# Optimization experiments

Hardware: AMD Instinct MI355X
Metric: run time of the kernel (lower is better)

Reference implementation:

```python
import jax, jax.numpy as jnp
import numpy as np

N_NODES = 100000
N_EDGES = 1600000
HIDDEN = 128
N_FILTERS = 64
CUTOFF = 8.0
BN_EPS = 1e-3  # keras BatchNormalization default epsilon


def setup_inputs() -> dict:
    key = jax.random.key(0)
    ks = jax.random.split(key, 12)
    x = jax.random.normal(ks[0], (N_NODES, HIDDEN), dtype=jnp.float32)
    edge_index = jax.random.randint(ks[1], (2, N_EDGES), 0, N_NODES, dtype=jnp.int32)
    edge_weight = jax.random.uniform(ks[2], (N_EDGES,), dtype=jnp.float32) * CUTOFF
    edge_attr = jax.random.uniform(ks[3], (N_EDGES, 1), dtype=jnp.float32)
    s = 0.05
    # filter_net: Dense(1->64, tanh), Dense(64->64)
    Wf1 = jax.random.normal(ks[4], (1, N_FILTERS), dtype=jnp.float32) * s
    bf1 = jnp.zeros((N_FILTERS,), jnp.float32)
    Wf2 = jax.random.normal(ks[5], (N_FILTERS, N_FILTERS), dtype=jnp.float32) * s
    bf2 = jnp.zeros((N_FILTERS,), jnp.float32)
    # interaction_net: Dense(128->128, softplus), Dense(128->128)
    Wi1 = jax.random.normal(ks[6], (HIDDEN, HIDDEN), dtype=jnp.float32) * s
    bi1 = jnp.zeros((HIDDEN,), jnp.float32)
    Wi2 = jax.random.normal(ks[7], (HIDDEN, HIDDEN), dtype=jnp.float32) * s
    bi2 = jnp.zeros((HIDDEN,), jnp.float32)
    # BatchNormalization (inference: moving stats)
    gamma = jnp.ones((HIDDEN,), jnp.float32)
    beta = jnp.zeros((HIDDEN,), jnp.float32)
    mov_mean = jax.random.normal(ks[8], (HIDDEN,), dtype=jnp.float32) * 0.01
    mov_var = jnp.ones((HIDDEN,), jnp.float32)
    return {"x": x, "edge_index": edge_index, "edge_weight": edge_weight,
            "edge_attr": edge_attr, "Wf1": Wf1, "bf1": bf1, "Wf2": Wf2, "bf2": bf2,
            "Wi1": Wi1, "bi1": bi1, "Wi2": Wi2, "bi2": bi2,
            "gamma": gamma, "beta": beta, "mov_mean": mov_mean, "mov_var": mov_var}


def reference(x, edge_index, edge_weight, edge_attr, Wf1, bf1, Wf2, bf2,
              Wi1, bi1, Wi2, bi2, gamma, beta, mov_mean, mov_var):
    row, col = edge_index[0], edge_index[1]
    # continuous filters with smooth cosine cutoff
    scaled = edge_weight * (2.0 / CUTOFF) - 1.0                    # [E]
    h = jnp.tanh(scaled[:, None] @ Wf1 + bf1)                      # [E, F]
    filters = h @ Wf2 + bf2                                        # [E, F]
    cut = 0.5 * (jnp.cos(edge_weight * jnp.pi / CUTOFF) + 1.0)
    cut = jnp.where(edge_weight <= CUTOFF, cut, 0.0)               # [E]
    filters = filters * cut[:, None]
    # Original: (neighbor[:, None, :] * filters[:, :, None]).sum(axis=1)
    # == neighbor * filters.sum(-1, keepdims) — same math, no [E,F,H] tensor.
    fsum = jnp.sum(filters, axis=-1, keepdims=True)                # [E, 1]
    messages = x[col] * fsum                                       # [E, H]
    agg = jax.ops.segment_sum(messages, row, num_segments=x.shape[0])  # [N, H]
    out = jax.nn.softplus(agg @ Wi1 + bi1) @ Wi2 + bi2             # [N, H]
    # BatchNormalization, inference mode (training=False)
    out = gamma * (out - mov_mean) * jax.lax.rsqrt(mov_var + BN_EPS) + beta
    return out
```

## Files before the change

### kernel.cpp

```cpp
#include <hip/hip_runtime.h>
#include <math.h>

#define HIDDEN 128
#define NFILT 64
#define SCAN_B 1024
#define LUTK 2048

typedef __attribute__((ext_vector_type(8))) short bf16x8;
typedef __attribute__((ext_vector_type(4))) float f32x4;

__device__ __forceinline__ short f2bf(float f) {
    unsigned u = __float_as_uint(f);
    unsigned r = (u + 0x7fffu + ((u >> 16) & 1u)) >> 16;
    return (short)r;
}
__device__ __forceinline__ float bf2f(unsigned short u) {
    return __uint_as_float(((unsigned)u) << 16);
}

__device__ __forceinline__ float softplus_fast(float v) {
    float e = __builtin_amdgcn_exp2f(v * 1.4426950408889634f);
    float r = 0.69314718055994531f * __builtin_amdgcn_logf(1.0f + e);
    return (v > 80.f) ? v : r;
}

__global__ void wsum_kernel(const float* __restrict__ Wf2, const float* __restrict__ bf2,
                            float* __restrict__ wsum, float* __restrict__ bsum) {
    int j = threadIdx.x;
    float s = 0.f;
    for (int f = 0; f < NFILT; ++f) s += Wf2[j * NFILT + f];
    wsum[j] = s;
    if (j == 0) {
        float b = 0.f;
        for (int f = 0; f < NFILT; ++f) b += bf2[f];
        *bsum = b;
    }
}

__device__ __forceinline__ float edge_coeff(float w,
                                            const float* sW, const float* sB,
                                            const float* sS, float bsum) {
    float s = fmaf(w, 0.25f, -1.0f);
    float acc = bsum;
    #pragma unroll 8
    for (int j = 0; j < NFILT; ++j)
        acc += tanhf(fmaf(s, sW[j], sB[j])) * sS[j];
    float cut = (w <= 8.0f) ? 0.5f * (cosf(w * 0.39269908169872414f) + 1.0f) : 0.0f;
    return acc * cut;
}

__global__ void lut_kernel(const float* __restrict__ Wf1, const float* __restrict__ bf1,
                           const float* __restrict__ wsum, const float* __restrict__ bsum,
                           float* __restrict__ lut) {
    int i = blockIdx.x * 256 + threadIdx.x;
    if (i > LUTK) return;
    float w = 8.0f * (float)i / (float)LUTK;
    lut[i] = edge_coeff(w, Wf1, bf1, wsum, *bsum);
}

__device__ __forceinline__ float lut_eval(const float* sl, float w) {
    float t = w * ((float)LUTK / 8.0f);
    t = fminf(fmaxf(t, 0.f), (float)LUTK);
    int i = (int)t;
    i = min(i, LUTK - 1);
    return fmaf(t - (float)i, sl[i + 1] - sl[i], sl[i]);
}

__global__ void prep_w_kernel(const float* __restrict__ Wi1, const float* __restrict__ Wi2,
                              short* __restrict__ W1T, short* __restrict__ W2T) {
    int idx = blockIdx.x * 256 + threadIdx.x;
    const float* src = (idx < 16384) ? Wi1 : Wi2;
    short* dst = (idx < 16384) ? W1T : W2T;
    int i = idx & 16383;
    int k = i >> 7, n = i & 127;
    dst[n * HIDDEN + k] = f2bf(src[i]);
}

__global__ void prep_bn_kernel(const float* __restrict__ bi2,
                               const float* __restrict__ gamma, const float* __restrict__ beta,
                               const float* __restrict__ mean, const float* __restrict__ var,
                               float* __restrict__ scf, float* __restrict__ shf) {
    int j = threadIdx.x;
    float sc = gamma[j] * rsqrtf(var[j] + 1e-3f);
    scf[j] = sc;
    shf[j] = (bi2[j] - mean[j]) * sc + beta[j];
}

__global__ void x2bf_kernel(const float* __restrict__ x, short* __restrict__ xh, int total8) {
    int i = blockIdx.x * 256 + threadIdx.x;
    if (i >= total8) return;
    const float4 v0 = *(const float4*)&x[(size_t)i * 8];
    const float4 v1 = *(const float4*)&x[(size_t)i * 8 + 4];
    bf16x8 o;
    o[0] = f2bf(v0.x); o[1] = f2bf(v0.y); o[2] = f2bf(v0.z); o[3] = f2bf(v0.w);
    o[4] = f2bf(v1.x); o[5] = f2bf(v1.y); o[6] = f2bf(v1.z); o[7] = f2bf(v1.w);
    *(bf16x8*)&xh[(size_t)i * 8] = o;
}

__global__ void count_rank_kernel(const int* __restrict__ rows, int* __restrict__ deg,
                                  int* __restrict__ rank, int E) {
    int e = blockIdx.x * blockDim.x + threadIdx.x;
    if (e < E) rank[e] = atomicAdd(&deg[rows[e]], 1);
}

__global__ void count_kernel(const int* __restrict__ rows, int* __restrict__ deg, int E) {
    int e = blockIdx.x * blockDim.x + threadIdx.x;
    if (e < E) atomicAdd(&deg[rows[e]], 1);
}

__global__ __launch_bounds__(SCAN_B) void scan_p1(const int* __restrict__ deg,
                                                  int* __restrict__ bsums, int N) {
    __shared__ int red[SCAN_B];
    int i = blockIdx.x * SCAN_B + threadIdx.x;
    red[threadIdx.x] = (i < N) ? deg[i] : 0;
    __syncthreads();
    for (int off = SCAN_B / 2; off > 0; off >>= 1) {
        if (threadIdx.x < off) red[threadIdx.x] += red[threadIdx.x + off];
        __syncthreads();
    }
    if (threadIdx.x == 0) bsums[blockIdx.x] = red[0];
}

__global__ __launch_bounds__(SCAN_B) void scan_p2(int* __restrict__ bsums, int B) {
    __shared__ int part[SCAN_B];
    int t = threadIdx.x;
    part[t] = (t < B) ? bsums[t] : 0;
    __syncthreads();
    for (int off = 1; off < SCAN_B; off <<= 1) {
        int v = (t >= off) ? part[t - off] : 0;
        __syncthreads();
        part[t] += v;
        __syncthreads();
    }
    if (t < B) bsums[t] = (t == 0) ? 0 : part[t - 1];
}

template <bool WRITE_CURSOR>
__global__ __launch_bounds__(SCAN_B) void scan_p3_t(int* __restrict__ deg,
                                                    const int* __restrict__ bsums,
                                                    int* __restrict__ offs, int N) {
    __shared__ int part[SCAN_B];
    int t = threadIdx.x;
    int i = blockIdx.x * SCAN_B + t;
    int d = (i < N) ? deg[i] : 0;
    part[t] = d;
    __syncthreads();
    for (int off = 1; off < SCAN_B; off <<= 1) {
        int v = (t >= off) ? part[t - off] : 0;
        __syncthreads();
        part[t] += v;
        __syncthreads();
    }
    int pre = bsums[blockIdx.x] + part[t] - d;
    if (i < N) {
        offs[i] = pre;
        if (WRITE_CURSOR) deg[i] = pre;
        if (i == N - 1) offs[N] = pre + d;
    }
}

__global__ __launch_bounds__(256) void fill_rank_kernel(
    const int* __restrict__ rows, const int* __restrict__ cols,
    const float* __restrict__ ew, const int* __restrict__ rank,
    const int* __restrict__ offs, const float* __restrict__ lut,
    int2* __restrict__ epack, int E) {
    __shared__ float sl[LUTK + 1];
    for (int i = threadIdx.x; i <= LUTK; i += 256) sl[i] = lut[i];
    __syncthreads();
    int e = blockIdx.x * 256 + threadIdx.x;
    if (e >= E) return;
    float f = lut_eval(sl, ew[e]);
    int pos = offs[rows[e]] + rank[e];
    epack[pos] = make_int2(cols[e], __float_as_int(f));
}

__global__ __launch_bounds__(256) void fill_cursor_kernel(
    const int* __restrict__ rows, const int* __restrict__ cols,
    const float* __restrict__ ew, int* __restrict__ cursor,
    const float* __restrict__ lut, int2* __restrict__ epack, int E) {
    __shared__ float sl[LUTK + 1];
    for (int i = threadIdx.x; i <= LUTK; i += 256) sl[i] = lut[i];
    __syncthreads();
    int e = blockIdx.x * 256 + threadIdx.x;
    if (e >= E) return;
    float f = lut_eval(sl, ew[e]);
    int pos = atomicAdd(&cursor[rows[e]], 1);
    epack[pos] = make_int2(cols[e], __float_as_int(f));
}

__global__ __launch_bounds__(256) void gather_bf_kernel(const int* __restrict__ offs,
                                                        const int2* __restrict__ epack,
                                                        const short* __restrict__ xh,
                                                        short* __restrict__ aggh, int N) {
    int t = threadIdx.x;
    int node = blockIdx.x * 8 + (t >> 5);
    if (node >= N) return;
    int lane = t & 31;
    int s = offs[node], eend = offs[node + 1];
    float a0 = 0.f, a1 = 0.f, a2 = 0.f, a3 = 0.f;

    int i = s;
    for (; i + 4 <= eend; i += 4) {
        int2 p0 = epack[i];
        int2 p1 = epack[i + 1];
        int2 p2 = epack[i + 2];
        int2 p3 = epack[i + 3];
        ushort4 x0 = *(const ushort4*)&xh[(size_t)p0.x * HIDDEN + lane * 4];
        ushort4 x1 = *(const ushort4*)&xh[(size_t)p1.x * HIDDEN + lane * 4];
        ushort4 x2 = *(const ushort4*)&xh[(size_t)p2.x * HIDDEN + lane * 4];
        ushort4 x3 = *(const ushort4*)&xh[(size_t)p3.x * HIDDEN + lane * 4];
        float f0 = __int_as_float(p0.y), f1 = __int_as_float(p1.y);
        float f2 = __int_as_float(p2.y), f3 = __int_as_float(p3.y);
        a0 = fmaf(bf2f(x0.x), f0, a0); a1 = fmaf(bf2f(x0.y), f0, a1);
        a2 = fmaf(bf2f(x0.z), f0, a2); a3 = fmaf(bf2f(x0.w), f0, a3);
        a0 = fmaf(bf2f(x1.x), f1, a0); a1 = fmaf(bf2f(x1.y), f1, a1);
        a2 = fmaf(bf2f(x1.z), f1, a2); a3 = fmaf(bf2f(x1.w), f1, a3);
        a0 = fmaf(bf2f(x2.x), f2, a0); a1 = fmaf(bf2f(x2.y), f2, a1);
        a2 = fmaf(bf2f(x2.z), f2, a2); a3 = fmaf(bf2f(x2.w), f2, a3);
        a0 = fmaf(bf2f(x3.x), f3, a0); a1 = fmaf(bf2f(x3.y), f3, a1);
        a2 = fmaf(bf2f(x3.z), f3, a2); a3 = fmaf(bf2f(x3.w), f3, a3);
    }
    for (; i < eend; ++i) {
        int2 p = epack[i];
        float f = __int_as_float(p.y);
        ushort4 xv = *(const ushort4*)&xh[(size_t)p.x * HIDDEN + lane * 4];
        a0 = fmaf(bf2f(xv.x), f, a0);
        a1 = fmaf(bf2f(xv.y), f, a1);
        a2 = fmaf(bf2f(xv.z), f, a2);
        a3 = fmaf(bf2f(xv.w), f, a3);
    }
    ushort4 o;
    o.x = (unsigned short)f2bf(a0);
    o.y = (unsigned short)f2bf(a1);
    o.z = (unsigned short)f2bf(a2);
    o.w = (unsigned short)f2bf(a3);
    *(ushort4*)&aggh[(size_t)node * HIDDEN + lane * 4] = o;
}

__global__ __launch_bounds__(256) void gather_kernel(const int* __restrict__ offs,
                                                     const int2* __restrict__ epack,
                                                     const float* __restrict__ x,
                                                     float* __restrict__ agg, int N) {
    int t = threadIdx.x;
    int node = blockIdx.x * 8 + (t >> 5);
    if (node >= N) return;
    int lane = t & 31;
    int s = offs[node], eend = offs[node + 1];
    float4 acc = make_float4(0.f, 0.f, 0.f, 0.f);
    int i = s;
    for (; i + 2 <= eend; i += 2) {
        int2 p0 = epack[i];
        int2 p1 = epack[i + 1];
        float4 x0 = *(const float4*)&x[(size_t)p0.x * HIDDEN + lane * 4];
        float4 x1 = *(const float4*)&x[(size_t)p1.x * HIDDEN + lane * 4];
        float f0 = __int_as_float(p0.y), f1 = __int_as_float(p1.y);
        acc.x = fmaf(x0.x, f0, acc.x); acc.y = fmaf(x0.y, f0, acc.y);
        acc.z = fmaf(x0.z, f0, acc.z); acc.w = fmaf(x0.w, f0, acc.w);
        acc.x = fmaf(x1.x, f1, acc.x); acc.y = fmaf(x1.y, f1, acc.y);
        acc.z = fmaf(x1.z, f1, acc.z); acc.w = fmaf(x1.w, f1, acc.w);
    }
    for (; i < eend; ++i) {
        int2 p = epack[i];
        float f = __int_as_float(p.y);
        const float4 xv = *(const float4*)&x[(size_t)p.x * HIDDEN + lane * 4];
        acc.x = fmaf(xv.x, f, acc.x);
        acc.y = fmaf(xv.y, f, acc.y);
        acc.z = fmaf(xv.z, f, acc.z);
        acc.w = fmaf(xv.w, f, acc.w);
    }
    *(float4*)&agg[(size_t)node * HIDDEN + lane * 4] = acc;
}

#define HROW 136

#define WSWZ(b) ((b) ^ ((((b) >> 8) & 7) << 4))

__global__ __launch_bounds__(512) void mlp_mfma_bf_kernel(
    const short* __restrict__ aggh, float* __restrict__ io,
    const short* __restrict__ W1T, const short* __restrict__ W2T,
    const float* __restrict__ bi1,
    const float* __restrict__ scf, const float* __restrict__ shf,
    int N) {
    __shared__ short wS[HIDDEN * HIDDEN];
    __shared__ short hS[128 * HROW];

    const int t = threadIdx.x;
    const int wave = t >> 6;
    const int lane = t & 63;
    const int quad = lane >> 4;
    const int m16  = lane & 15;
    const int row0 = blockIdx.x * 128 + wave * 16;
    const int arow = row0 + m16;

    const int swzmask = (m16 & 7) << 4;

    bf16x8 w2r[4];
    {
        const bf16x8* w1v = (const bf16x8*)W1T;
        const bf16x8* w2v = (const bf16x8*)W2T;
        bf16x8 w1r[4];
        #pragma unroll
        for (int j = 0; j < 4; ++j) w1r[j] = w1v[t + 512 * j];
        #pragma unroll
        for (int j = 0; j < 4; ++j) w2r[j] = w2v[t + 512 * j];
        #pragma unroll
        for (int j = 0; j < 4; ++j) {
            int b = (t + 512 * j) * 16;
            *(bf16x8*)((char*)wS + WSWZ(b)) = w1r[j];
        }
    }

    float b1v[8];
    #pragma unroll
    for (int ct = 0; ct < 8; ++ct) b1v[ct] = bi1[ct * 16 + m16];

    f32x4 acc[8];
    #pragma unroll
    for (int ct = 0; ct < 8; ++ct) acc[ct] = (f32x4)(0.f);

    __syncthreads();

    #pragma unroll
    for (int ks = 0; ks < 4; ++ks) {
        bf16x8 a;
        if (arow < N) {
            a = *(const bf16x8*)&aggh[(size_t)arow * HIDDEN + ks * 32 + quad * 8];
        } else {
            #pragma unroll
            for (int j = 0; j < 8; ++j) a[j] = 0;
        }
        const char* bbase = (const char*)wS + m16 * 256 + ((ks * 64 + quad * 16) ^ swzmask);
        #pragma unroll
        for (int ct = 0; ct < 8; ++ct) {
            bf16x8 b = *(const bf16x8*)(bbase + ct * 4096);
            acc[ct] = __builtin_amdgcn_mfma_f32_16x16x32_bf16(a, b, acc[ct], 0, 0, 0);
        }
    }

    #pragma unroll
    for (int ct = 0; ct < 8; ++ct) {
        int col = ct * 16 + m16;
        #pragma unroll
        for (int r = 0; r < 4; ++r) {
            int lrow = wave * 16 + quad * 4 + r;
            float h = softplus_fast(acc[ct][r] + b1v[ct]);
            hS[lrow * HROW + col] = f2bf(h);
        }
        acc[ct] = (f32x4)(0.f);
    }
    __syncthreads();

    #pragma unroll
    for (int j = 0; j < 4; ++j) {
        int b = (t + 512 * j) * 16;
        *(bf16x8*)((char*)wS + WSWZ(b)) = w2r[j];
    }
    __syncthreads();

    float scv[8], shv[8];
    #pragma unroll
    for (int ct = 0; ct < 8; ++ct) {
        scv[ct] = scf[ct * 16 + m16];
        shv[ct] = shf[ct * 16 + m16];
    }

    #pragma unroll
    for (int ks = 0; ks < 4; ++ks) {
        bf16x8 a = *(const bf16x8*)&hS[(wave * 16 + m16) * HROW + ks * 32 + quad * 8];
        const char* bbase = (const char*)wS + m16 * 256 + ((ks * 64 + quad * 16) ^ swzmask);
        #pragma unroll
        for (int ct = 0; ct < 8; ++ct) {
            bf16x8 b = *(const bf16x8*)(bbase + ct * 4096);
            acc[ct] = __builtin_amdgcn_mfma_f32_16x16x32_bf16(a, b, acc[ct], 0, 0, 0);
        }
    }

    #pragma unroll
    for (int r = 0; r < 4; ++r) {
        int grow = row0 + quad * 4 + r;
        if (grow < N) {
            float* p = &io[(size_t)grow * HIDDEN + m16];
            #pragma unroll
            for (int ct = 0; ct < 8; ++ct)
                p[ct * 16] = fmaf(acc[ct][r], scv[ct], shv[ct]);
        }
    }
}

__global__ __launch_bounds__(256) void mlp_mfma_kernel(
    float* io,
    const short* __restrict__ W1T, const short* __restrict__ W2T,
    const float* __restrict__ bi1,
    const float* __restrict__ scf, const float* __restrict__ shf,
    int N) {
    __shared__ short hS[64 * HROW];

    const int t = threadIdx.x;
    const int wave = t >> 6;
    const int lane = t & 63;
    const int quad = lane >> 4;
    const int m16  = lane & 15;
    const int row0 = blockIdx.x * 64 + wave * 16;
    const int arow = row0 + m16;

    f32x4 acc[8];
    #pragma unroll
    for (int ct = 0; ct < 8; ++ct) acc[ct] = (f32x4)(0.f);

    #pragma unroll
    for (int ks = 0; ks < 4; ++ks) {
        bf16x8 a;
        if (arow < N) {
            const float* ap = &io[(size_t)arow * HIDDEN + ks * 32 + quad * 8];
            float4 v0 = *(const float4*)ap;
            float4 v1 = *(const float4*)(ap + 4);
            a[0] = f2bf(v0.x); a[1] = f2bf(v0.y); a[2] = f2bf(v0.z); a[3] = f2bf(v0.w);
            a[4] = f2bf(v1.x); a[5] = f2bf(v1.y); a[6] = f2bf(v1.z); a[7] = f2bf(v1.w);
        } else {
            #pragma unroll
            for (int j = 0; j < 8; ++j) a[j] = 0;
        }
        #pragma unroll
        for (int ct = 0; ct < 8; ++ct) {
            bf16x8 b = *(const bf16x8*)&W1T[(ct * 16 + m16) * HIDDEN + ks * 32 + quad * 8];
            acc[ct] = __builtin_amdgcn_mfma_f32_16x16x32_bf16(a, b, acc[ct], 0, 0, 0);
        }
    }

    #pragma unroll
    for (int ct = 0; ct < 8; ++ct) {
        int col = ct * 16 + m16;
        float b1 = bi1[col];
        #pragma unroll
        for (int r = 0; r < 4; ++r) {
            int lrow = wave * 16 + quad * 4 + r;
            float h = softplus_fast(acc[ct][r] + b1);
            hS[lrow * HROW + col] = f2bf(h);
            acc[ct][r] = 0.f;
        }
    }
    __syncthreads();

    #pragma unroll
    for (int ks = 0; ks < 4; ++ks) {
        bf16x8 a = *(const bf16x8*)&hS[(wave * 16 + m16) * HROW + ks * 32 + quad * 8];
        #pragma unroll
        for (int ct = 0; ct < 8; ++ct) {
            bf16x8 b = *(const bf16x8*)&W2T[(ct * 16 + m16) * HIDDEN + ks * 32 + quad * 8];
            acc[ct] = __builtin_amdgcn_mfma_f32_16x16x32_bf16(a, b, acc[ct], 0, 0, 0);
        }
    }

    #pragma unroll
    for (int ct = 0; ct < 8; ++ct) {
        int col = ct * 16 + m16;
        float sc = scf[col], sh = shf[col];
        #pragma unroll
        for (int r = 0; r < 4; ++r) {
            int grow = row0 + quad * 4 + r;
            if (grow < N)
                io[(size_t)grow * HIDDEN + col] = fmaf(acc[ct][r], sc, sh);
        }
    }
}

__global__ void edge_filter_kernel(const float* __restrict__ ew,
                                   const float* __restrict__ Wf1, const float* __restrict__ bf1,
                                   const float* __restrict__ wsum, const float* __restrict__ bsum,
                                   float* __restrict__ fs, int E) {
    __shared__ float sW[NFILT], sB[NFILT], sS[NFILT];
    if (threadIdx.x < NFILT) {
        sW[threadIdx.x] = Wf1[threadIdx.x];
        sB[threadIdx.x] = bf1[threadIdx.x];
        sS[threadIdx.x] = wsum[threadIdx.x];
    }
    __syncthreads();
    int e = blockIdx.x * blockDim.x + threadIdx.x;
    if (e >= E) return;
    fs[e] = edge_coeff(ew[e], sW, sB, sS, *bsum);
}

__global__ void scatter_kernel(const int* __restrict__ rows, const int* __restrict__ cols,
                               const float* __restrict__ x, const float* __restrict__ fs,
                               float* __restrict__ agg, int E) {
    int t = threadIdx.x;
    int e = blockIdx.x * 8 + (t >> 5);
    if (e >= E) return;
    int lane = t & 31;
    int r = rows[e];
    int c = cols[e];
    float f = fs[e];
    const float4 xv = *(const float4*)&x[c * HIDDEN + lane * 4];
    float* dst = &agg[r * HIDDEN + lane * 4];
    atomicAdd(dst + 0, xv.x * f);
    atomicAdd(dst + 1, xv.y * f);
    atomicAdd(dst + 2, xv.z * f);
    atomicAdd(dst + 3, xv.w * f);
}

__global__ __launch_bounds__(256) void mlp_kernel(
    float* __restrict__ io,
    const float* __restrict__ Wi1, const float* __restrict__ bi1,
    const float* __restrict__ Wi2, const float* __restrict__ bi2,
    const float* __restrict__ gamma, const float* __restrict__ beta,
    const float* __restrict__ mean, const float* __restrict__ var,
    int N) {
    __shared__ float As[64 * HIDDEN];
    __shared__ float Wh[64 * HIDDEN];

    const int t = threadIdx.x;
    const int row0 = blockIdx.x * 64;
    const int col4 = (t & 31) * 4;
    const int rgrp = t >> 5;

    #pragma unroll
    for (int i = 0; i < 8; ++i) {
        int f4 = t + 256 * i;
        int r = f4 >> 5, c4 = (f4 & 31) * 4;
        int node = row0 + r;
        float4 v = make_float4(0.f, 0.f, 0.f, 0.f);
        if (node < N) v = *(const float4*)&io[node * HIDDEN + c4];
        *(float4*)&As[r * HIDDEN + c4] = v;
    }

    float acc[8][4];
    #pragma unroll
    for (int r = 0; r < 8; ++r)
        for (int j = 0; j < 4; ++j) acc[r][j] = 0.f;

    for (int kh = 0; kh < 2; ++kh) {
        __syncthreads();
        #pragma unroll
        for (int i = 0; i < 8; ++i) {
            int f4 = t + 256 * i;
            int kr = f4 >> 5, c4 = (f4 & 31) * 4;
            *(float4*)&Wh[kr * HIDDEN + c4] = *(const float4*)&Wi1[(kh * 64 + kr) * HIDDEN + c4];
        }
        __syncthreads();
        for (int k = 0; k < 64; ++k) {
            float4 w = *(const float4*)&Wh[k * HIDDEN + col4];
            #pragma unroll
            for (int r = 0; r < 8; ++r) {
                float a = As[(rgrp + 8 * r) * HIDDEN + kh * 64 + k];
                acc[r][0] = fmaf(a, w.x, acc[r][0]);
                acc[r][1] = fmaf(a, w.y, acc[r][1]);
                acc[r][2] = fmaf(a, w.z, acc[r][2]);
                acc[r][3] = fmaf(a, w.w, acc[r][3]);
            }
        }
    }
    __syncthreads();

    {
        float4 b = *(const float4*)&bi1[col4];
        float bv[4] = {b.x, b.y, b.z, b.w};
        #pragma unroll
        for (int r = 0; r < 8; ++r) {
            float hv[4];
            #pragma unroll
            for (int j = 0; j < 4; ++j) {
                float v = acc[r][j] + bv[j];
                hv[j] = softplus_fast(v);
                acc[r][j] = 0.f;
            }
            *(float4*)&As[(rgrp + 8 * r) * HIDDEN + col4] =
                make_float4(hv[0], hv[1], hv[2], hv[3]);
        }
    }

    for (int kh = 0; kh < 2; ++kh) {
        __syncthreads();
        #pragma unroll
        for (int i = 0; i < 8; ++i) {
            int f4 = t + 256 * i;
            int kr = f4 >> 5, c4 = (f4 & 31) * 4;
            *(float4*)&Wh[kr * HIDDEN + c4] = *(const float4*)&Wi2[(kh * 64 + kr) * HIDDEN + c4];
        }
        __syncthreads();
        for (int k = 0; k < 64; ++k) {
            float4 w = *(const float4*)&Wh[k * HIDDEN + col4];
            #pragma unroll
            for (int r = 0; r < 8; ++r) {
                float a = As[(rgrp + 8 * r) * HIDDEN + kh * 64 + k];
                acc[r][0] = fmaf(a, w.x, acc[r][0]);
                acc[r][1] = fmaf(a, w.y, acc[r][1]);
                acc[r][2] = fmaf(a, w.z, acc[r][2]);
                acc[r][3] = fmaf(a, w.w, acc[r][3]);
            }
        }
    }

    {
        float4 b2 = *(const float4*)&bi2[col4];
        float4 g  = *(const float4*)&gamma[col4];
        float4 be = *(const float4*)&beta[col4];
        float4 mu = *(const float4*)&mean[col4];
        float4 va = *(const float4*)&var[col4];
        float bv[4]  = {b2.x, b2.y, b2.z, b2.w};
        float gv[4]  = {g.x, g.y, g.z, g.w};
        float bev[4] = {be.x, be.y, be.z, be.w};
        float muv[4] = {mu.x, mu.y, mu.z, mu.w};
        float vav[4] = {va.x, va.y, va.z, va.w};
        float sc[4];
        #pragma unroll
        for (int j = 0; j < 4; ++j) sc[j] = gv[j] * rsqrtf(vav[j] + 1e-3f);
        #pragma unroll
        for (int r = 0; r < 8; ++r) {
            int node = row0 + rgrp + 8 * r;
            if (node < N) {
                float o[4];
                #pragma unroll
                for (int j = 0; j < 4; ++j)
                    o[j] = (acc[r][j] + bv[j] - muv[j]) * sc[j] + bev[j];
                *(float4*)&io[node * HIDDEN + col4] = make_float4(o[0], o[1], o[2], o[3]);
            }
        }
    }
}

extern "C" void kernel_launch(void* const* d_in, const int* in_sizes, int n_in,
                              void* d_out, int out_size, void* d_ws, size_t ws_size,
                              hipStream_t stream) {
    const float* x    = (const float*)d_in[0];
    const int*   ei   = (const int*)d_in[1];
    const float* ew   = (const float*)d_in[2];
    const float* Wf1  = (const float*)d_in[4];
    const float* bf1  = (const float*)d_in[5];
    const float* Wf2  = (const float*)d_in[6];
    const float* bf2  = (const float*)d_in[7];
    const float* Wi1  = (const float*)d_in[8];
    const float* bi1  = (const float*)d_in[9];
    const float* Wi2  = (const float*)d_in[10];
    const float* bi2  = (const float*)d_in[11];
    const float* gam  = (const float*)d_in[12];
    const float* bet  = (const float*)d_in[13];
    const float* mmu  = (const float*)d_in[14];
    const float* mva  = (const float*)d_in[15];

    const int N = in_sizes[0] / HIDDEN;
    const int E = in_sizes[2];
    const int* rows = ei;
    const int* cols = ei + E;

    float* io = (float*)d_out;

    const int B = (N + SCAN_B - 1) / SCAN_B;

    char* ws = (char*)d_ws;
    int*   deg    = (int*)ws;
    int*   offs   = deg + N;
    int*   bsums  = offs + N + 1;
    float* wsumv  = (float*)(bsums + B);
    float* bsumv  = wsumv + NFILT;
    float* lut    = bsumv + 1;
    size_t hdr_ints  = (size_t)(2 * N + 1 + B + NFILT + 1 + LUTK + 1);
    size_t epack_off = ((hdr_ints * 4) + 15) & ~(size_t)15;
    int2*  epack  = (int2*)(ws + epack_off);
    size_t wT_off = (epack_off + (size_t)E * sizeof(int2) + 15) & ~(size_t)15;
    short* W1T    = (short*)(ws + wT_off);
    short* W2T    = W1T + HIDDEN * HIDDEN;
    float* scf    = (float*)(W2T + HIDDEN * HIDDEN);
    float* shf    = scf + HIDDEN;
    size_t base_need = wT_off + 2 * HIDDEN * HIDDEN * sizeof(short) + 2 * HIDDEN * sizeof(float);
    size_t rank_off  = (base_need + 15) & ~(size_t)15;
    int*   rank   = (int*)(ws + rank_off);
    size_t rank_need = rank_off + (size_t)E * sizeof(int);
    size_t xh_off    = (rank_need + 15) & ~(size_t)15;
    short* xh     = (short*)(ws + xh_off);
    short* aggh   = xh + (size_t)N * HIDDEN;
    size_t bf_need = xh_off + 2 * (size_t)N * HIDDEN * sizeof(short);

    if (ws_size >= base_need && B <= SCAN_B) {
        const bool use_rank = (ws_size >= rank_need);
        const bool use_bf   = (ws_size >= bf_need);
        hipMemsetAsync(deg, 0, (size_t)N * sizeof(int), stream);
        wsum_kernel<<<1, 64, 0, stream>>>(Wf2, bf2, wsumv, bsumv);
        lut_kernel<<<(LUTK + 256) / 256, 256, 0, stream>>>(Wf1, bf1, wsumv, bsumv, lut);
        prep_w_kernel<<<128, 256, 0, stream>>>(Wi1, Wi2, W1T, W2T);
        prep_bn_kernel<<<1, HIDDEN, 0, stream>>>(bi2, gam, bet, mmu, mva, scf, shf);
        if (use_bf) {
            int total8 = N * (HIDDEN / 8);
            x2bf_kernel<<<(total8 + 255) / 256, 256, 0, stream>>>(x, xh, total8);
        }
        if (use_rank)
            count_rank_kernel<<<(E + 255) / 256, 256, 0, stream>>>(rows, deg, rank, E);
        else
            count_kernel<<<(E + 255) / 256, 256, 0, stream>>>(rows, deg, E);
        scan_p1<<<B, SCAN_B, 0, stream>>>(deg, bsums, N);
        scan_p2<<<1, SCAN_B, 0, stream>>>(bsums, B);
        if (use_rank) {
            scan_p3_t<false><<<B, SCAN_B, 0, stream>>>(deg, bsums, offs, N);
            fill_rank_kernel<<<(E + 255) / 256, 256, 0, stream>>>(rows, cols, ew, rank,
                                                                  offs, lut, epack, E);
        } else {
            scan_p3_t<true><<<B, SCAN_B, 0, stream>>>(deg, bsums, offs, N);
            fill_cursor_kernel<<<(E + 255) / 256, 256, 0, stream>>>(rows, cols, ew, deg,
                                                                    lut, epack, E);
        }
        if (use_bf) {
            gather_bf_kernel<<<(N + 7) / 8, 256, 0, stream>>>(offs, epack, xh, aggh, N);
            mlp_mfma_bf_kernel<<<(N + 127) / 128, 512, 0, stream>>>(aggh, io, W1T, W2T,
                                                                    bi1, scf, shf, N);
        } else {
            gather_kernel<<<(N + 7) / 8, 256, 0, stream>>>(offs, epack, x, io, N);
            mlp_mfma_kernel<<<(N + 63) / 64, 256, 0, stream>>>(io, W1T, W2T, bi1, scf, shf, N);
        }
    } else {
        float* fs = (float*)d_ws;
        float* w2 = fs + E;
        float* b2 = w2 + NFILT;
        hipMemsetAsync(d_out, 0, (size_t)out_size * sizeof(float), stream);
        wsum_kernel<<<1, 64, 0, stream>>>(Wf2, bf2, w2, b2);
        edge_filter_kernel<<<(E + 255) / 256, 256, 0, stream>>>(ew, Wf1, bf1, w2, b2, fs, E);
        scatter_kernel<<<(E + 7) / 8, 256, 0, stream>>>(rows, cols, x, fs, io, E);
        mlp_kernel<<<(N + 63) / 64, 256, 0, stream>>>(io, Wi1, bi1, Wi2, bi2,
                                                      gam, bet, mmu, mva, N);
    }
}
```

Before: 367.4 us.

## Fuse prep kernels, merge bf16 conversion with degree count, widen gather vectors

Merges the wsum, BN-prep and weight-transpose kernels into one launch, and fuses the x-to-bf16 conversion with the degree counting/ranking pass to cut launch count and overlap memory streams. The bf16 gather now uses 16 lanes per node with 16-byte loads (8 bf16 per lane), processing 16 nodes per block instead of 8. The fused x2bf/count kernel assumes use_bf implies use_rank, which holds given the workspace layout; the wider gather loads may change memory-level parallelism per node.

```diff
diff --git a/kernel.cpp b/kernel.cpp
--- a/kernel.cpp
+++ b/kernel.cpp
@@ -67,34 +67,53 @@
 }
 
 __global__ void prep_w_kernel(const float* __restrict__ Wi1, const float* __restrict__ Wi2,
-                              short* __restrict__ W1T, short* __restrict__ W2T) {
+                              short* __restrict__ W1T, short* __restrict__ W2T,
+                              const float* __restrict__ Wf2, const float* __restrict__ bf2,
+                              float* __restrict__ wsum, float* __restrict__ bsum,
+                              const float* __restrict__ bi2,
+                              const float* __restrict__ gamma, const float* __restrict__ beta,
+                              const float* __restrict__ mean, const float* __restrict__ var,
+                              float* __restrict__ scf, float* __restrict__ shf) {
     int idx = blockIdx.x * 256 + threadIdx.x;
     const float* src = (idx < 16384) ? Wi1 : Wi2;
     short* dst = (idx < 16384) ? W1T : W2T;
     int i = idx & 16383;
     int k = i >> 7, n = i & 127;
     dst[n * HIDDEN + k] = f2bf(src[i]);
-}
-
-__global__ void prep_bn_kernel(const float* __restrict__ bi2,
-                               const float* __restrict__ gamma, const float* __restrict__ beta,
-                               const float* __restrict__ mean, const float* __restrict__ var,
-                               float* __restrict__ scf, float* __restrict__ shf) {
-    int j = threadIdx.x;
-    float sc = gamma[j] * rsqrtf(var[j] + 1e-3f);
-    scf[j] = sc;
-    shf[j] = (bi2[j] - mean[j]) * sc + beta[j];
-}
-
-__global__ void x2bf_kernel(const float* __restrict__ x, short* __restrict__ xh, int total8) {
+
+    if (blockIdx.x == 0 && threadIdx.x < 64) {
+        int j = threadIdx.x;
+        float s = 0.f;
+        for (int f = 0; f < NFILT; ++f) s += Wf2[j * NFILT + f];
+        wsum[j] = s;
+        if (j == 0) {
+            float b = 0.f;
+            for (int f = 0; f < NFILT; ++f) b += bf2[f];
+            *bsum = b;
+        }
+    }
+    if (blockIdx.x == 1 && threadIdx.x < HIDDEN) {
+        int j = threadIdx.x;
+        float sc = gamma[j] * rsqrtf(var[j] + 1e-3f);
+        scf[j] = sc;
+        shf[j] = (bi2[j] - mean[j]) * sc + beta[j];
+    }
+}
+
+__global__ __launch_bounds__(256) void x2bf_count_kernel(
+    const float* __restrict__ x, short* __restrict__ xh, int total8,
+    const int* __restrict__ rows, int* __restrict__ deg,
+    int* __restrict__ rank, int E) {
     int i = blockIdx.x * 256 + threadIdx.x;
-    if (i >= total8) return;
-    const float4 v0 = *(const float4*)&x[(size_t)i * 8];
-    const float4 v1 = *(const float4*)&x[(size_t)i * 8 + 4];
-    bf16x8 o;
-    o[0] = f2bf(v0.x); o[1] = f2bf(v0.y); o[2] = f2bf(v0.z); o[3] = f2bf(v0.w);
-    o[4] = f2bf(v1.x); o[5] = f2bf(v1.y); o[6] = f2bf(v1.z); o[7] = f2bf(v1.w);
-    *(bf16x8*)&xh[(size_t)i * 8] = o;
+    if (i < E) rank[i] = atomicAdd(&deg[rows[i]], 1);
+    if (i < total8) {
+        const float4 v0 = *(const float4*)&x[(size_t)i * 8];
+        const float4 v1 = *(const float4*)&x[(size_t)i * 8 + 4];
+        bf16x8 o;
+        o[0] = f2bf(v0.x); o[1] = f2bf(v0.y); o[2] = f2bf(v0.z); o[3] = f2bf(v0.w);
+        o[4] = f2bf(v1.x); o[5] = f2bf(v1.y); o[6] = f2bf(v1.z); o[7] = f2bf(v1.w);
+        *(bf16x8*)&xh[(size_t)i * 8] = o;
+    }
 }
 
 __global__ void count_rank_kernel(const int* __restrict__ rows, int* __restrict__ deg,
@@ -193,11 +212,14 @@
                                                         const short* __restrict__ xh,
                                                         short* __restrict__ aggh, int N) {
     int t = threadIdx.x;
-    int node = blockIdx.x * 8 + (t >> 5);
+    int node = blockIdx.x * 16 + (t >> 4);
     if (node >= N) return;
-    int lane = t & 31;
+    int lane = t & 15;
     int s = offs[node], eend = offs[node + 1];
-    float a0 = 0.f, a1 = 0.f, a2 = 0.f, a3 = 0.f;
+
+    float a[8];
+    #pragma unroll
+    for (int j = 0; j < 8; ++j) a[j] = 0.f;
 
     int i = s;
     for (; i + 4 <= eend; i += 4) {
@@ -205,36 +227,33 @@
         int2 p1 = epack[i + 1];
         int2 p2 = epack[i + 2];
         int2 p3 = epack[i + 3];
-        ushort4 x0 = *(const ushort4*)&xh[(size_t)p0.x * HIDDEN + lane * 4];
-        ushort4 x1 = *(const ushort4*)&xh[(size_t)p1.x * HIDDEN + lane * 4];
-        ushort4 x2 = *(const ushort4*)&xh[(size_t)p2.x * HIDDEN + lane * 4];
-        ushort4 x3 = *(const ushort4*)&xh[(size_t)p3.x * HIDDEN + lane * 4];
+        bf16x8 x0 = *(const bf16x8*)&xh[(size_t)p0.x * HIDDEN + lane * 8];
+        bf16x8 x1 = *(const bf16x8*)&xh[(size_t)p1.x * HIDDEN + lane * 8];
+        bf16x8 x2 = *(const bf16x8*)&xh[(size_t)p2.x * HIDDEN + lane * 8];
+        bf16x8 x3 = *(const bf16x8*)&xh[(size_t)p3.x * HIDDEN + lane * 8];
         float f0 = __int_as_float(p0.y), f1 = __int_as_float(p1.y);
         float f2 = __int_as_float(p2.y), f3 = __int_as_float(p3.y);
-        a0 = fmaf(bf2f(x0.x), f0, a0); a1 = fmaf(bf2f(x0.y), f0, a1);
-        a2 = fmaf(bf2f(x0.z), f0, a2); a3 = fmaf(bf2f(x0.w), f0, a3);
-        a0 = fmaf(bf2f(x1.x), f1, a0); a1 = fmaf(bf2f(x1.y), f1, a1);
-        a2 = fmaf(bf2f(x1.z), f1, a2); a3 = fmaf(bf2f(x1.w), f1, a3);
-        a0 = fmaf(bf2f(x2.x), f2, a0); a1 = fmaf(bf2f(x2.y), f2, a1);
-        a2 = fmaf(bf2f(x2.z), f2, a2); a3 = fmaf(bf2f(x2.w), f2, a3);
-        a0 = fmaf(bf2f(x3.x), f3, a0); a1 = fmaf(bf2f(x3.y), f3, a1);
-        a2 = fmaf(bf2f(x3.z), f3, a2); a3 = fmaf(bf2f(x3.w), f3, a3);
+        #pragma unroll
+        for (int j = 0; j < 8; ++j) a[j] = fmaf(bf2f((unsigned short)x0[j]), f0, a[j]);
+        #pragma unroll
+        for (int j = 0; j < 8; ++j) a[j] = fmaf(bf2f((unsigned short)x1[j]), f1, a[j]);
+        #pragma unroll
+        for (int j = 0; j < 8; ++j) a[j] = fmaf(bf2f((unsigned short)x2[j]), f2, a[j]);
+        #pragma unroll
+        for (int j = 0; j < 8; ++j) a[j] = fmaf(bf2f((unsigned short)x3[j]), f3, a[j]);
     }
     for (; i < eend; ++i) {
         int2 p = epack[i];
         float f = __int_as_float(p.y);
-        ushort4 xv = *(const ushort4*)&xh[(size_t)p.x * HIDDEN + lane * 4];
-        a0 = fmaf(bf2f(xv.x), f, a0);
-        a1 = fmaf(bf2f(xv.y), f, a1);
-        a2 = fmaf(bf2f(xv.z), f, a2);
-        a3 = fmaf(bf2f(xv.w), f, a3);
-    }
-    ushort4 o;
-    o.x = (unsigned short)f2bf(a0);
-    o.y = (unsigned short)f2bf(a1);
-    o.z = (unsigned short)f2bf(a2);
-    o.w = (unsigned short)f2bf(a3);
-    *(ushort4*)&aggh[(size_t)node * HIDDEN + lane * 4] = o;
+        bf16x8 xv = *(const bf16x8*)&xh[(size_t)p.x * HIDDEN + lane * 8];
+        #pragma unroll
+        for (int j = 0; j < 8; ++j) a[j] = fmaf(bf2f((unsigned short)xv[j]), f, a[j]);
+    }
+
+    bf16x8 o;
+    #pragma unroll
+    for (int j = 0; j < 8; ++j) o[j] = f2bf(a[j]);
+    *(bf16x8*)&aggh[(size_t)node * HIDDEN + lane * 8] = o;
 }
 
 __global__ __launch_bounds__(256) void gather_kernel(const int* __restrict__ offs,
@@ -674,18 +693,20 @@
         const bool use_rank = (ws_size >= rank_need);
         const bool use_bf   = (ws_size >= bf_need);
         hipMemsetAsync(deg, 0, (size_t)N * sizeof(int), stream);
-        wsum_kernel<<<1, 64, 0, stream>>>(Wf2, bf2, wsumv, bsumv);
+        prep_w_kernel<<<128, 256, 0, stream>>>(Wi1, Wi2, W1T, W2T,
+                                               Wf2, bf2, wsumv, bsumv,
+                                               bi2, gam, bet, mmu, mva, scf, shf);
         lut_kernel<<<(LUTK + 256) / 256, 256, 0, stream>>>(Wf1, bf1, wsumv, bsumv, lut);
-        prep_w_kernel<<<128, 256, 0, stream>>>(Wi1, Wi2, W1T, W2T);
-        prep_bn_kernel<<<1, HIDDEN, 0, stream>>>(bi2, gam, bet, mmu, mva, scf, shf);
         if (use_bf) {
             int total8 = N * (HIDDEN / 8);
-            x2bf_kernel<<<(total8 + 255) / 256, 256, 0, stream>>>(x, xh, total8);
-        }
-        if (use_rank)
+            int work = (total8 > E) ? total8 : E;
+            x2bf_count_kernel<<<(work + 255) / 256, 256, 0, stream>>>(x, xh, total8,
+                                                                      rows, deg, rank, E);
+        } else if (use_rank) {
             count_rank_kernel<<<(E + 255) / 256, 256, 0, stream>>>(rows, deg, rank, E);
-        else
+        } else {
             count_kernel<<<(E + 255) / 256, 256, 0, stream>>>(rows, deg, E);
+        }
         scan_p1<<<B, SCAN_B, 0, stream>>>(deg, bsums, N);
         scan_p2<<<1, SCAN_B, 0, stream>>>(bsums, B);
         if (use_rank) {
@@ -698,7 +719,7 @@
                                                                     lut, epack, E);
         }
         if (use_bf) {
-            gather_bf_kernel<<<(N + 7) / 8, 256, 0, stream>>>(offs, epack, xh, aggh, N);
+            gather_bf_kernel<<<(N + 15) / 16, 256, 0, stream>>>(offs, epack, xh, aggh, N);
             mlp_mfma_bf_kernel<<<(N + 127) / 128, 512, 0, stream>>>(aggh, io, W1T, W2T,
                                                                     bi1, scf, shf, N);
         } else {
```

Result: faster. 353.1 us (-3.9%).
